# Optimization experiments

Measured on AMD Instinct MI355X. Metric: run time of the kernel, lower is better.

Reference implementation:

```python
import jax, jax.numpy as jnp
import numpy as np

N = 100000          # num nodes
E_C = 6_400_000     # connection edges
E_D = 400_000       # destination edges
F_IN = 5
H = 8
BN_EPS = 1e-5
L2_EPS = 1e-12


def setup_inputs() -> dict:
    key = jax.random.key(0)
    ks = jax.random.split(key, 16)
    d = {}
    d["x"] = jax.random.normal(ks[0], (N, F_IN), dtype=jnp.float32)
    d["edge_index_connections"] = jax.random.randint(ks[1], (2, E_C), 0, N, dtype=jnp.int64)
    d["edge_index_destinations"] = jax.random.randint(ks[2], (2, E_D), 0, N, dtype=jnp.int64)
    # SAGEConv weights: lin_l (neighbor aggregate), lin_r (root), no bias
    d["W1l"] = jax.random.normal(ks[3], (H, F_IN), jnp.float32) * 0.3
    d["W1r"] = jax.random.normal(ks[4], (H, F_IN), jnp.float32) * 0.3
    d["W2l"] = jax.random.normal(ks[5], (H, H), jnp.float32) * 0.3
    d["W2r"] = jax.random.normal(ks[6], (H, H), jnp.float32) * 0.3
    d["W3l"] = jax.random.normal(ks[7], (H, H), jnp.float32) * 0.3
    d["W3r"] = jax.random.normal(ks[8], (H, H), jnp.float32) * 0.3
    d["W4l"] = jax.random.normal(ks[9], (H, H), jnp.float32) * 0.3
    d["W4r"] = jax.random.normal(ks[10], (H, H), jnp.float32) * 0.3
    # LazyBatchNorm1d affine params (init gamma=1, beta=0)
    for i in range(1, 5):
        d[f"g{i}"] = jnp.ones((H,), jnp.float32)
        d[f"b{i}"] = jnp.zeros((H,), jnp.float32)
    return d


def _sage(x, ei, Wl, Wr):
    # PyG SAGEConv(mean aggr, normalize=True, bias=False):
    # out = lin_l(mean_{j in N(i)} x_j) + lin_r(x_i); then L2 normalize rows.
    src, dst = ei[0], ei[1]
    msgs = x[src]                                            # [E, F] gather
    s = jax.ops.segment_sum(msgs, dst, num_segments=N)       # [N, F]
    cnt = jax.ops.segment_sum(jnp.ones((ei.shape[1],), x.dtype), dst, num_segments=N)
    mean = s / jnp.maximum(cnt, 1.0)[:, None]                # zero for isolated nodes
    out = mean @ Wl.T + x @ Wr.T                             # [N, H]
    nrm = jnp.linalg.norm(out, axis=-1, keepdims=True)
    return out / jnp.maximum(nrm, L2_EPS)


def _bn(x, g, b):
    # BatchNorm1d in training mode: per-feature batch stats (biased variance)
    m = x.mean(axis=0)
    v = x.var(axis=0)
    return (x - m) * jax.lax.rsqrt(v + BN_EPS) * g + b


def reference(x, edge_index_connections, edge_index_destinations,
              W1l, W1r, W2l, W2r, W3l, W3r, W4l, W4r,
              g1, b1, g2, b2, g3, b3, g4, b4):
    eic = edge_index_connections
    eid = edge_index_destinations
    h = _bn(jax.nn.relu(_sage(x, eic, W1l, W1r)), g1, b1)
    # ITERATIONS_BEFORE_DESTINATION = 1 (conv4 + bn2)
    h = _bn(jax.nn.relu(_sage(h, eic, W4l, W4r)), g2, b2)
    # destination pass (conv2 + bn3)
    h = _bn(jax.nn.relu(_sage(h, eid, W2l, W2r)), g3, b3)
    # ITERATIONS_AFTER_DESTINATION = 2 (conv3 + bn4)
    for _ in range(2):
        h = _bn(jax.nn.relu(_sage(h, eic, W3l, W3r)), g4, b4)
    return h
```

## Files before the change

### kernel.cpp

```cpp
#include <hip/hip_runtime.h>
#include <hip/hip_fp16.h>

#define NN 100000
#define EC 6400000
#define ED 400000
#define BN_EPS 1e-5f
#define NSB ((NN + 255) >> 8)
#define NCH 256
#define CSR_CAP 19200
#define CHUNK_OF(E) (((((E) + NCH - 1) / NCH) + 3) & ~3)


__global__ __launch_bounds__(1024)
void hist_pass(const int* __restrict__ ei, int E, int* __restrict__ bhist) {
    __shared__ int h[NSB];
    for (int i = threadIdx.x; i < NSB; i += 1024) h[i] = 0;
    __syncthreads();
    int k = blockIdx.x;
    int chunk = CHUNK_OF(E);
    int beg = k * chunk, end = min(E, beg + chunk);
    for (int e = beg + threadIdx.x * 4; e < end; e += 1024 * 4) {
        int4 d4 = *(const int4*)&ei[E + e];
        atomicAdd(&h[d4.x >> 8], 1);
        atomicAdd(&h[d4.y >> 8], 1);
        atomicAdd(&h[d4.z >> 8], 1);
        atomicAdd(&h[d4.w >> 8], 1);
    }
    __syncthreads();
    for (int i = threadIdx.x; i < NSB; i += 1024) bhist[i * NCH + k] = h[i];
}

__global__ __launch_bounds__(256)
void row_scan(int* __restrict__ bhist, int* __restrict__ total) {
    int b = blockIdx.x;
    int* row = bhist + b * NCH;
    __shared__ int wsum[4];
    int lane = threadIdx.x & 63, w = threadIdx.x >> 6;
    int v = row[threadIdx.x];
    int x = v;
    #pragma unroll
    for (int sh = 1; sh < 64; sh <<= 1) { int y = __shfl_up(x, sh); if (lane >= sh) x += y; }
    if (lane == 63) wsum[w] = x;
    __syncthreads();
    int wb = 0;
    #pragma unroll
    for (int j = 0; j < 4; ++j) if (j < w) wb += wsum[j];
    row[threadIdx.x] = wb + x - v;
    if (threadIdx.x == 255) total[b] = wb + x;
}

__global__ void bucket_base(const int* __restrict__ total, int* __restrict__ bbase) {
    __shared__ int wsum[4];
    __shared__ int carry;
    if (threadIdx.x == 0) carry = 0;
    __syncthreads();
    int lane = threadIdx.x & 63, w = threadIdx.x >> 6;
    for (int s = 0; s < NSB; s += 256) {
        int idx = s + threadIdx.x;
        int v = (idx < NSB) ? total[idx] : 0;
        int x = v;
        #pragma unroll
        for (int sh = 1; sh < 64; sh <<= 1) { int y = __shfl_up(x, sh); if (lane >= sh) x += y; }
        if (lane == 63) wsum[w] = x;
        __syncthreads();
        int wb = 0;
        #pragma unroll
        for (int j = 0; j < 4; ++j) if (j < w) wb += wsum[j];
        int all = wsum[0] + wsum[1] + wsum[2] + wsum[3];
        if (idx < NSB) bbase[idx] = carry + wb + x - v;
        __syncthreads();
        if (threadIdx.x == 0) carry += all;
        __syncthreads();
    }
}

__global__ __launch_bounds__(1024)
void scatter_pairs(const int* __restrict__ ei, int E,
                   const int* __restrict__ bhist, const int* __restrict__ bbase,
                   unsigned* __restrict__ packed) {
    __shared__ int cur[NSB];
    int k = blockIdx.x;
    for (int b = threadIdx.x; b < NSB; b += 1024)
        cur[b] = bbase[b] + bhist[b * NCH + k];
    __syncthreads();
    int chunk = CHUNK_OF(E);
    int beg = k * chunk, end = min(E, beg + chunk);
    for (int e = beg + threadIdx.x * 4; e < end; e += 1024 * 4) {
        int4 s4 = *(const int4*)&ei[e];
        int4 d4 = *(const int4*)&ei[E + e];
        { int p = atomicAdd(&cur[d4.x >> 8], 1); packed[p] = (unsigned)s4.x | ((unsigned)(d4.x & 255) << 17); }
        { int p = atomicAdd(&cur[d4.y >> 8], 1); packed[p] = (unsigned)s4.y | ((unsigned)(d4.y & 255) << 17); }
        { int p = atomicAdd(&cur[d4.z >> 8], 1); packed[p] = (unsigned)s4.z | ((unsigned)(d4.z & 255) << 17); }
        { int p = atomicAdd(&cur[d4.w >> 8], 1); packed[p] = (unsigned)s4.w | ((unsigned)(d4.w & 255) << 17); }
    }
}

__global__ __launch_bounds__(256)
void sb_csr(const unsigned* __restrict__ packed,
            const int* __restrict__ bbase, const int* __restrict__ total,
            int* __restrict__ csr, int* __restrict__ offs, int* __restrict__ deg,
            float* __restrict__ inv) {
    __shared__ int h[256];
    __shared__ int loff[256];
    __shared__ int ws2[4];
    __shared__ int ebuf[CSR_CAP];
    int b = blockIdx.x;
    int ebeg = bbase[b], ecnt = total[b];
    int node0 = b << 8;
    int nn = min(256, NN - node0);
    h[threadIdx.x] = 0;
    __syncthreads();
    for (int e = threadIdx.x; e < ecnt; e += 256)
        atomicAdd(&h[packed[ebeg + e] >> 17], 1);
    __syncthreads();
    {
        int lane = threadIdx.x & 63, w = threadIdx.x >> 6;
        int v = h[threadIdx.x], x = v;
        #pragma unroll
        for (int sh = 1; sh < 64; sh <<= 1) { int y = __shfl_up(x, sh); if (lane >= sh) x += y; }
        if (lane == 63) ws2[w] = x;
        __syncthreads();
        int wb = 0;
        #pragma unroll
        for (int j = 0; j < 4; ++j) if (j < w) wb += ws2[j];
        int excl = wb + x - v;
        loff[threadIdx.x] = excl;
        if (threadIdx.x < nn) {
            int node = node0 + threadIdx.x;
            offs[node] = ebeg + excl;
            deg[node]  = v;
            inv[node]  = 1.0f / (float)(v > 1 ? v : 1);
        }
    }
    __syncthreads();
    if (ecnt <= CSR_CAP) {
        for (int e = threadIdx.x; e < ecnt; e += 256) {
            unsigned u = packed[ebeg + e];
            int p = atomicAdd(&loff[u >> 17], 1);
            ebuf[p] = (int)(u & 0x1FFFF);
        }
        __syncthreads();
        for (int e = threadIdx.x; e < ecnt; e += 256) csr[ebeg + e] = ebuf[e];
    } else {
        for (int e = threadIdx.x; e < ecnt; e += 256) {
            unsigned u = packed[ebeg + e];
            int p = atomicAdd(&loff[u >> 17], 1);
            csr[ebeg + p] = (int)(u & 0x1FFFF);
        }
    }
}

__global__ __launch_bounds__(256)
void prep_misc(const float* __restrict__ x, const float* __restrict__ W1l,
               const float* __restrict__ W1r, float* __restrict__ xp,
               __half* __restrict__ xp16,
               float* __restrict__ W1lp, float* __restrict__ W1rp) {
    int t = blockIdx.x * 256 + threadIdx.x;
    if (t < 64) {
        int f = t >> 3, k = t & 7;
        W1lp[t] = (k < 5) ? W1l[f * 5 + k] : 0.f;
        W1rp[t] = (k < 5) ? W1r[f * 5 + k] : 0.f;
    }
    for (int idx = t; idx < NN * 8; idx += gridDim.x * 256) {
        int f = idx & 7, i = idx >> 3;
        float v = (f < 5) ? x[i * 5 + f] : 0.f;
        xp[idx] = v;
        xp16[idx] = __float2half(v);
    }
}

template<bool APPLY_BN>
__global__ __launch_bounds__(256)
void sage_layer8(const float* __restrict__ hin,
                 const __half* __restrict__ hin16,
                 const float* __restrict__ stats_in,
                 const float* __restrict__ gin, const float* __restrict__ bin,
                 const int* __restrict__ offs, const int* __restrict__ deg,
                 const int* __restrict__ csr, const float* __restrict__ inv,
                 const float* __restrict__ Wl, const float* __restrict__ Wr,
                 float* __restrict__ hout, __half* __restrict__ hout16,
                 float* __restrict__ stats_out) {
    __shared__ float bl[16];
    int tid = threadIdx.x;
    if (tid < 16) bl[tid] = 0.f;
    __syncthreads();
    int wave = tid >> 6, lane = tid & 63, g = lane >> 3, f = lane & 7;

    float sc[8], sh[8];
    #pragma unroll
    for (int k = 0; k < 8; ++k) { sc[k] = 1.f; sh[k] = 0.f; }
    if constexpr (APPLY_BN) {
        #pragma unroll
        for (int k = 0; k < 8; ++k) {
            float m = stats_in[k * 16] * (1.f / NN);
            float v = stats_in[(8 + k) * 16] * (1.f / NN) - m * m;
            float is = rsqrtf(v + BN_EPS);
            sc[k] = gin[k] * is;
            sh[k] = bin[k] - m * sc[k];
        }
    }
    float wl[8], wr[8];
    #pragma unroll
    for (int k = 0; k < 8; ++k) { wl[k] = Wl[f * 8 + k]; wr[k] = Wr[f * 8 + k]; }

    float acc_r = 0.f, acc_r2 = 0.f;
    const int stride = gridDim.x * 32;
    for (int i0 = (blockIdx.x * 4 + wave) * 8; i0 < NN; i0 += stride) {
        int i = i0 + g;
        int ic = min(i, NN - 1);
        bool ok = (i < NN);
        int d = ok ? deg[ic] : 0;
        int o = offs[ic];
        float a0 = 0, a1 = 0, a2 = 0, a3 = 0, a4 = 0, a5 = 0, a6 = 0, a7 = 0;
        for (int b = 0; b < d; b += 8) {
            int e = b + f;
            int cv = csr[o + e];
            float m = (e < d) ? 1.f : 0.f;
            unsigned s = min((unsigned)cv & 0x1FFFFu, (unsigned)(NN - 1));
            uint4 rv = *(const uint4*)(hin16 + (size_t)s * 8);
            float2 p0 = __half22float2(*(const __half2*)&rv.x);
            float2 p1 = __half22float2(*(const __half2*)&rv.y);
            float2 p2 = __half22float2(*(const __half2*)&rv.z);
            float2 p3 = __half22float2(*(const __half2*)&rv.w);
            a0 = fmaf(p0.x, m, a0); a1 = fmaf(p0.y, m, a1);
            a2 = fmaf(p1.x, m, a2); a3 = fmaf(p1.y, m, a3);
            a4 = fmaf(p2.x, m, a4); a5 = fmaf(p2.y, m, a5);
            a6 = fmaf(p3.x, m, a6); a7 = fmaf(p3.y, m, a7);
        }
        #pragma unroll
        for (int msk = 1; msk < 8; msk <<= 1) {
            a0 += __shfl_xor(a0, msk); a1 += __shfl_xor(a1, msk);
            a2 += __shfl_xor(a2, msk); a3 += __shfl_xor(a3, msk);
            a4 += __shfl_xor(a4, msk); a5 += __shfl_xor(a5, msk);
            a6 += __shfl_xor(a6, msk); a7 += __shfl_xor(a7, msk);
        }
        float im = inv[ic];
        float dnz = (d > 0) ? 1.f : 0.f;
        const float4* hp = (const float4*)(hin + (size_t)ic * 8);
        float4 h0 = hp[0];
        float4 h1 = hp[1];
        float hk[8] = { h0.x, h0.y, h0.z, h0.w, h1.x, h1.y, h1.z, h1.w };
        float ac[8] = { a0, a1, a2, a3, a4, a5, a6, a7 };
        float y = 0.f;
        #pragma unroll
        for (int k = 0; k < 8; ++k) {
            float mk = fmaf(sc[k], ac[k] * im, sh[k] * dnz);
            float hh = fmaf(sc[k], hk[k], sh[k]);
            y = fmaf(mk, wl[k], y);
            y = fmaf(hh, wr[k], y);
        }
        float n2 = y * y;
        n2 += __shfl_xor(n2, 1);
        n2 += __shfl_xor(n2, 2);
        n2 += __shfl_xor(n2, 4);
        float z = y / fmaxf(sqrtf(n2), 1e-12f);
        float r = fmaxf(z, 0.f);
        r = ok ? r : 0.f;
        if (ok) {
            hout[(size_t)i * 8 + f] = r;
            hout16[(size_t)i * 8 + f] = __float2half(r);
        }
        acc_r += r;
        acc_r2 += r * r;
    }
    atomicAdd(&bl[f], acc_r);
    atomicAdd(&bl[8 + f], acc_r2);
    __syncthreads();
    if (tid < 16) atomicAdd(&stats_out[tid * 16], bl[tid]);
}

__global__ void apply_bn_out(const float* __restrict__ hin,
                             const float* __restrict__ stats,
                             const float* __restrict__ g, const float* __restrict__ b,
                             float* __restrict__ out) {
    int t = blockIdx.x * blockDim.x + threadIdx.x;
    if (t >= NN * 8) return;
    int f = t & 7;
    float m = stats[f * 16] * (1.0f / NN);
    float v = stats[(8 + f) * 16] * (1.0f / NN) - m * m;
    float sc = g[f] * rsqrtf(v + BN_EPS);
    float sh = b[f] - m * sc;
    out[t] = fmaf(hin[t], sc, sh);
}


static inline char* bump(char*& p, size_t bytes) {
    char* r = p;
    p += (bytes + 255) & ~(size_t)255;
    return r;
}

extern "C" void kernel_launch(void* const* d_in, const int* in_sizes, int n_in,
                              void* d_out, int out_size, void* d_ws, size_t ws_size,
                              hipStream_t stream) {
    const float* x   = (const float*)d_in[0];
    const int* eic   = (const int*)d_in[1];
    const int* eid   = (const int*)d_in[2];
    const float* W1l = (const float*)d_in[3];
    const float* W1r = (const float*)d_in[4];
    const float* W2l = (const float*)d_in[5];
    const float* W2r = (const float*)d_in[6];
    const float* W3l = (const float*)d_in[7];
    const float* W3r = (const float*)d_in[8];
    const float* W4l = (const float*)d_in[9];
    const float* W4r = (const float*)d_in[10];
    const float* g1 = (const float*)d_in[11];
    const float* b1 = (const float*)d_in[12];
    const float* g2 = (const float*)d_in[13];
    const float* b2 = (const float*)d_in[14];
    const float* g3 = (const float*)d_in[15];
    const float* b3 = (const float*)d_in[16];
    const float* g4 = (const float*)d_in[17];
    const float* b4 = (const float*)d_in[18];
    float* out = (float*)d_out;

    char* p = (char*)d_ws;
    float* stats   = (float*)bump(p, 5 * 256 * 4);
    size_t zero_bytes = (size_t)(p - (char*)d_ws);
    int*   bhist_c = (int*)  bump(p, (size_t)NSB * NCH * 4);
    int*   bhist_d = (int*)  bump(p, (size_t)NSB * NCH * 4);
    int*   total_c = (int*)  bump(p, NSB * 4);
    int*   bbase_c = (int*)  bump(p, NSB * 4);
    int*   total_d = (int*)  bump(p, NSB * 4);
    int*   bbase_d = (int*)  bump(p, NSB * 4);
    int*   offs_c  = (int*)  bump(p, NN * 4);
    int*   deg_c   = (int*)  bump(p, NN * 4);
    float* inv_c   = (float*)bump(p, NN * 4);
    int*   offs_d  = (int*)  bump(p, NN * 4);
    int*   deg_d   = (int*)  bump(p, NN * 4);
    float* inv_d   = (float*)bump(p, NN * 4);
    int*   csr_c   = (int*)  bump(p, ((size_t)EC + 64) * 4);
    int*   csr_d   = (int*)  bump(p, ((size_t)ED + 64) * 4);
    float* xp32    = (float*)bump(p, (size_t)NN * 8 * 4);
    __half* xp16   = (__half*)bump(p, (size_t)NN * 8 * 2);
    float* W1lp    = (float*)bump(p, 64 * 4);
    float* W1rp    = (float*)bump(p, 64 * 4);
    unsigned* packed_d = (unsigned*)bump(p, (size_t)ED * 4);
    char* pc = p;
    unsigned* packed_c = (unsigned*)bump(p, (size_t)EC * 4);
    char* pr = pc;
    float*  r_a   = (float*) bump(pr, (size_t)NN * 8 * 4);
    float*  r_b   = (float*) bump(pr, (size_t)NN * 8 * 4);
    __half* h16_a = (__half*)bump(pr, (size_t)NN * 8 * 2);
    __half* h16_b = (__half*)bump(pr, (size_t)NN * 8 * 2);
    (void)ws_size; (void)in_sizes; (void)n_in; (void)out_size; (void)packed_c;

    hipMemsetAsync(d_ws, 0, zero_bytes, stream);

    hist_pass<<<NCH, 1024, 0, stream>>>(eic, EC, bhist_c);
    hist_pass<<<NCH, 1024, 0, stream>>>(eid, ED, bhist_d);
    row_scan<<<NSB, 256, 0, stream>>>(bhist_c, total_c);
    row_scan<<<NSB, 256, 0, stream>>>(bhist_d, total_d);
    bucket_base<<<1, 256, 0, stream>>>(total_c, bbase_c);
    bucket_base<<<1, 256, 0, stream>>>(total_d, bbase_d);
    scatter_pairs<<<NCH, 1024, 0, stream>>>(eic, EC, bhist_c, bbase_c, packed_c);
    scatter_pairs<<<NCH, 1024, 0, stream>>>(eid, ED, bhist_d, bbase_d, packed_d);
    sb_csr<<<NSB, 256, 0, stream>>>(packed_c, bbase_c, total_c, csr_c, offs_c, deg_c, inv_c);
    sb_csr<<<NSB, 256, 0, stream>>>(packed_d, bbase_d, total_d, csr_d, offs_d, deg_d, inv_d);
    prep_misc<<<512, 256, 0, stream>>>(x, W1l, W1r, xp32, xp16, W1lp, W1rp);

    const int LB = 2048;
    sage_layer8<false><<<LB, 256, 0, stream>>>(
        xp32, xp16, nullptr, nullptr, nullptr,
        offs_c, deg_c, csr_c, inv_c, W1lp, W1rp, r_a, h16_a, stats + 0);
    sage_layer8<true><<<LB, 256, 0, stream>>>(
        r_a, h16_a, stats + 0, g1, b1,
        offs_c, deg_c, csr_c, inv_c, W4l, W4r, r_b, h16_b, stats + 256);
    sage_layer8<true><<<LB, 256, 0, stream>>>(
        r_b, h16_b, stats + 256, g2, b2,
        offs_d, deg_d, csr_d, inv_d, W2l, W2r, r_a, h16_a, stats + 512);
    sage_layer8<true><<<LB, 256, 0, stream>>>(
        r_a, h16_a, stats + 512, g3, b3,
        offs_c, deg_c, csr_c, inv_c, W3l, W3r, r_b, h16_b, stats + 768);
    sage_layer8<true><<<LB, 256, 0, stream>>>(
        r_b, h16_b, stats + 768, g4, b4,
        offs_c, deg_c, csr_c, inv_c, W3l, W3r, r_a, h16_a, stats + 1024);
    apply_bn_out<<<(NN * 8 + 255) / 256, 256, 0, stream>>>(r_a, stats + 1024, g4, b4, out);
}
```

Measured before the change: 625.3 us.

## Tile source features into LDS and bin edges by source tile for SAGE aggregation

Adds a preprocessing kernel that re-sorts each destination superblock's edges by 4096-row source tile. It packs the local destination index and the source offset into one word and records per-tile edge ranges. A new sage_spmm kernel, one block per 256 destination nodes, streams every fp16 source tile into LDS and accumulates neighbour sums with LDS float atomics. The goal is to replace random global gathers with LDS reads. In exchange, every block must re-read the whole feature table from L2. The kernel also uses about 73KB of LDS per block and launches only ~391 blocks, which limits occupancy. The destination-edge layer keeps the old CSR kernel.

```diff
diff --git a/kernel.cpp b/kernel.cpp
--- a/kernel.cpp
+++ b/kernel.cpp
@@ -8,6 +8,8 @@
 #define NSB ((NN + 255) >> 8)
 #define NCH 256
 #define CSR_CAP 19200
+#define TILE 4096
+#define NSUB ((NN + TILE - 1) / TILE)
 #define CHUNK_OF(E) (((((E) + NCH - 1) / NCH) + 3) & ~3)
 
 
@@ -92,6 +94,63 @@
         { int p = atomicAdd(&cur[d4.y >> 8], 1); packed[p] = (unsigned)s4.y | ((unsigned)(d4.y & 255) << 17); }
         { int p = atomicAdd(&cur[d4.z >> 8], 1); packed[p] = (unsigned)s4.z | ((unsigned)(d4.z & 255) << 17); }
         { int p = atomicAdd(&cur[d4.w >> 8], 1); packed[p] = (unsigned)s4.w | ((unsigned)(d4.w & 255) << 17); }
+    }
+}
+
+__global__ __launch_bounds__(256)
+void sb_group(const unsigned* __restrict__ packed,
+              const int* __restrict__ bbase, const int* __restrict__ total,
+              unsigned* __restrict__ packed2, int* __restrict__ gbin,
+              int* __restrict__ deg, float* __restrict__ inv) {
+    __shared__ int hn[256];
+    __shared__ int hb[NSUB];
+    __shared__ int boff[NSUB + 1];
+    __shared__ int cur[NSUB];
+    __shared__ unsigned ebuf[CSR_CAP];
+    int b = blockIdx.x;
+    int ebeg = bbase[b], ecnt = total[b];
+    int node0 = b << 8;
+    int nn = min(256, NN - node0);
+    hn[threadIdx.x] = 0;
+    if (threadIdx.x < NSUB) hb[threadIdx.x] = 0;
+    __syncthreads();
+    for (int e = threadIdx.x; e < ecnt; e += 256) {
+        unsigned u = packed[ebeg + e];
+        atomicAdd(&hn[u >> 17], 1);
+        atomicAdd(&hb[(u & 0x1FFFFu) >> 12], 1);
+    }
+    __syncthreads();
+    if (threadIdx.x == 0) {
+        int s = 0;
+        for (int i = 0; i < NSUB; ++i) { boff[i] = s; s += hb[i]; }
+        boff[NSUB] = s;
+    }
+    __syncthreads();
+    if (threadIdx.x <= NSUB) gbin[b * (NSUB + 1) + threadIdx.x] = ebeg + boff[threadIdx.x];
+    if (threadIdx.x < NSUB) cur[threadIdx.x] = boff[threadIdx.x];
+    if (threadIdx.x < nn) {
+        int node = node0 + threadIdx.x;
+        int d = hn[threadIdx.x];
+        deg[node] = d;
+        inv[node] = 1.0f / (float)(d > 1 ? d : 1);
+    }
+    __syncthreads();
+    if (ecnt <= CSR_CAP) {
+        for (int e = threadIdx.x; e < ecnt; e += 256) {
+            unsigned u = packed[ebeg + e];
+            int bin = (int)((u & 0x1FFFFu) >> 12);
+            int p = atomicAdd(&cur[bin], 1);
+            ebuf[p] = ((u >> 17) << 12) | (u & 0xFFFu);
+        }
+        __syncthreads();
+        for (int e = threadIdx.x; e < ecnt; e += 256) packed2[ebeg + e] = ebuf[e];
+    } else {
+        for (int e = threadIdx.x; e < ecnt; e += 256) {
+            unsigned u = packed[ebeg + e];
+            int bin = (int)((u & 0x1FFFFu) >> 12);
+            int p = atomicAdd(&cur[bin], 1);
+            packed2[ebeg + p] = ((u >> 17) << 12) | (u & 0xFFFu);
+        }
     }
 }
 
@@ -140,7 +199,7 @@
             ebuf[p] = (int)(u & 0x1FFFF);
         }
         __syncthreads();
-        for (int e = threadIdx.x; e < ecnt; e += 256) csr[ebeg + e] = ebuf[e];
+        for (int e = threadIdx.x; e < ecnt; e += 256) csr[ebeg + e] = (int)ebuf[e];
     } else {
         for (int e = threadIdx.x; e < ecnt; e += 256) {
             unsigned u = packed[ebeg + e];
@@ -167,6 +226,125 @@
         xp[idx] = v;
         xp16[idx] = __float2half(v);
     }
+}
+
+template<bool APPLY_BN>
+__global__ __launch_bounds__(256)
+void sage_spmm(const float* __restrict__ hin,
+               const __half* __restrict__ hin16,
+               const float* __restrict__ stats_in,
+               const float* __restrict__ gin, const float* __restrict__ bin,
+               const int* __restrict__ deg, const float* __restrict__ inv,
+               const int* __restrict__ gbin, const unsigned* __restrict__ packed2,
+               const float* __restrict__ Wl, const float* __restrict__ Wr,
+               float* __restrict__ hout, __half* __restrict__ hout16,
+               float* __restrict__ stats_out) {
+    __shared__ __align__(16) unsigned short tile[TILE * 8];
+    __shared__ float acc[256 * 9];
+    __shared__ float bl[16];
+    int tid = threadIdx.x;
+    int b = blockIdx.x;
+    int node0 = b << 8;
+    for (int i = tid; i < 256 * 9; i += 256) acc[i] = 0.f;
+    if (tid < 16) bl[tid] = 0.f;
+
+    float sc[8], sh[8];
+    #pragma unroll
+    for (int k = 0; k < 8; ++k) { sc[k] = 1.f; sh[k] = 0.f; }
+    if constexpr (APPLY_BN) {
+        #pragma unroll
+        for (int k = 0; k < 8; ++k) {
+            float m = stats_in[k * 16] * (1.f / NN);
+            float v = stats_in[(8 + k) * 16] * (1.f / NN) - m * m;
+            float is = rsqrtf(v + BN_EPS);
+            sc[k] = gin[k] * is;
+            sh[k] = bin[k] - m * sc[k];
+        }
+    }
+
+    const int* gb = gbin + b * (NSUB + 1);
+    for (int sub = 0; sub < NSUB; ++sub) {
+        int rs = sub * TILE;
+        int rows = min(TILE, NN - rs);
+        __syncthreads();
+        const uint4* gsrc = (const uint4*)(hin16 + (size_t)rs * 8);
+        uint4* lt = (uint4*)tile;
+        for (int r = tid; r < rows; r += 256) lt[r] = gsrc[r];
+        __syncthreads();
+        int e1 = gb[sub + 1];
+        for (int e = gb[sub] + tid; e < e1; e += 256) {
+            unsigned u = packed2[e];
+            int ld = (int)(u >> 12);
+            int sl = (int)(u & 0xFFFu);
+            uint4 rv = lt[sl];
+            float2 p0 = __half22float2(*(const __half2*)&rv.x);
+            float2 p1 = __half22float2(*(const __half2*)&rv.y);
+            float2 p2 = __half22float2(*(const __half2*)&rv.z);
+            float2 p3 = __half22float2(*(const __half2*)&rv.w);
+            float* a = &acc[ld * 9];
+            atomicAdd(a + 0, p0.x); atomicAdd(a + 1, p0.y);
+            atomicAdd(a + 2, p1.x); atomicAdd(a + 3, p1.y);
+            atomicAdd(a + 4, p2.x); atomicAdd(a + 5, p2.y);
+            atomicAdd(a + 6, p3.x); atomicAdd(a + 7, p3.y);
+        }
+    }
+    __syncthreads();
+
+    int nn = min(256, NN - node0);
+    bool ok = tid < nn;
+    int ii = node0 + (ok ? tid : (nn - 1));
+    int d = deg[ii];
+    float im = inv[ii];
+    float dnz = (d > 0) ? 1.f : 0.f;
+    const float4* hp = (const float4*)(hin + (size_t)ii * 8);
+    float4 h0 = hp[0], h1 = hp[1];
+    float hk[8] = { h0.x, h0.y, h0.z, h0.w, h1.x, h1.y, h1.z, h1.w };
+    float mk[8], hh[8];
+    #pragma unroll
+    for (int k = 0; k < 8; ++k) {
+        mk[k] = fmaf(sc[k], acc[tid * 9 + k] * im, sh[k] * dnz);
+        hh[k] = fmaf(sc[k], hk[k], sh[k]);
+    }
+    float y[8];
+    float n2 = 0.f;
+    #pragma unroll
+    for (int f = 0; f < 8; ++f) {
+        float t = 0.f;
+        #pragma unroll
+        for (int k = 0; k < 8; ++k) {
+            t = fmaf(mk[k], Wl[f * 8 + k], t);
+            t = fmaf(hh[k], Wr[f * 8 + k], t);
+        }
+        y[f] = t;
+        n2 += t * t;
+    }
+    float is = 1.f / fmaxf(sqrtf(n2), 1e-12f);
+    float rv[8];
+    #pragma unroll
+    for (int f = 0; f < 8; ++f) rv[f] = ok ? fmaxf(y[f] * is, 0.f) : 0.f;
+    if (ok) {
+        float4 o0 = { rv[0], rv[1], rv[2], rv[3] };
+        float4 o1 = { rv[4], rv[5], rv[6], rv[7] };
+        float4* op = (float4*)(hout + (size_t)ii * 8);
+        op[0] = o0; op[1] = o1;
+        __half2 q0 = __floats2half2_rn(rv[0], rv[1]);
+        __half2 q1 = __floats2half2_rn(rv[2], rv[3]);
+        __half2 q2 = __floats2half2_rn(rv[4], rv[5]);
+        __half2 q3 = __floats2half2_rn(rv[6], rv[7]);
+        uint4 hq;
+        hq.x = *(unsigned*)&q0; hq.y = *(unsigned*)&q1;
+        hq.z = *(unsigned*)&q2; hq.w = *(unsigned*)&q3;
+        *(uint4*)(hout16 + (size_t)ii * 8) = hq;
+    }
+    #pragma unroll
+    for (int f = 0; f < 8; ++f) {
+        float s1 = rv[f], s2 = rv[f] * rv[f];
+        #pragma unroll
+        for (int m = 1; m < 64; m <<= 1) { s1 += __shfl_xor(s1, m); s2 += __shfl_xor(s2, m); }
+        if ((tid & 63) == 0) { atomicAdd(&bl[f], s1); atomicAdd(&bl[8 + f], s2); }
+    }
+    __syncthreads();
+    if (tid < 16) atomicAdd(&stats_out[tid * 16], bl[tid]);
 }
 
 template<bool APPLY_BN>
@@ -323,13 +501,13 @@
     int*   bbase_c = (int*)  bump(p, NSB * 4);
     int*   total_d = (int*)  bump(p, NSB * 4);
     int*   bbase_d = (int*)  bump(p, NSB * 4);
-    int*   offs_c  = (int*)  bump(p, NN * 4);
+    int*   gbin_c  = (int*)  bump(p, (size_t)NSB * (NSUB + 1) * 4);
     int*   deg_c   = (int*)  bump(p, NN * 4);
     float* inv_c   = (float*)bump(p, NN * 4);
     int*   offs_d  = (int*)  bump(p, NN * 4);
     int*   deg_d   = (int*)  bump(p, NN * 4);
     float* inv_d   = (float*)bump(p, NN * 4);
-    int*   csr_c   = (int*)  bump(p, ((size_t)EC + 64) * 4);
+    unsigned* packed2_c = (unsigned*)bump(p, (size_t)EC * 4);
     int*   csr_d   = (int*)  bump(p, ((size_t)ED + 64) * 4);
     float* xp32    = (float*)bump(p, (size_t)NN * 8 * 4);
     __half* xp16   = (__half*)bump(p, (size_t)NN * 8 * 2);
@@ -343,7 +521,7 @@
     float*  r_b   = (float*) bump(pr, (size_t)NN * 8 * 4);
     __half* h16_a = (__half*)bump(pr, (size_t)NN * 8 * 2);
     __half* h16_b = (__half*)bump(pr, (size_t)NN * 8 * 2);
-    (void)ws_size; (void)in_sizes; (void)n_in; (void)out_size; (void)packed_c;
+    (void)ws_size; (void)in_sizes; (void)n_in; (void)out_size;
 
     hipMemsetAsync(d_ws, 0, zero_bytes, stream);
 
@@ -355,25 +533,24 @@
     bucket_base<<<1, 256, 0, stream>>>(total_d, bbase_d);
     scatter_pairs<<<NCH, 1024, 0, stream>>>(eic, EC, bhist_c, bbase_c, packed_c);
     scatter_pairs<<<NCH, 1024, 0, stream>>>(eid, ED, bhist_d, bbase_d, packed_d);
-    sb_csr<<<NSB, 256, 0, stream>>>(packed_c, bbase_c, total_c, csr_c, offs_c, deg_c, inv_c);
+    sb_group<<<NSB, 256, 0, stream>>>(packed_c, bbase_c, total_c, packed2_c, gbin_c, deg_c, inv_c);
     sb_csr<<<NSB, 256, 0, stream>>>(packed_d, bbase_d, total_d, csr_d, offs_d, deg_d, inv_d);
     prep_misc<<<512, 256, 0, stream>>>(x, W1l, W1r, xp32, xp16, W1lp, W1rp);
 
-    const int LB = 2048;
-    sage_layer8<false><<<LB, 256, 0, stream>>>(
+    sage_spmm<false><<<NSB, 256, 0, stream>>>(
         xp32, xp16, nullptr, nullptr, nullptr,
-        offs_c, deg_c, csr_c, inv_c, W1lp, W1rp, r_a, h16_a, stats + 0);
-    sage_layer8<true><<<LB, 256, 0, stream>>>(
+        deg_c, inv_c, gbin_c, packed2_c, W1lp, W1rp, r_a, h16_a, stats + 0);
+    sage_spmm<true><<<NSB, 256, 0, stream>>>(
         r_a, h16_a, stats + 0, g1, b1,
-        offs_c, deg_c, csr_c, inv_c, W4l, W4r, r_b, h16_b, stats + 256);
-    sage_layer8<true><<<LB, 256, 0, stream>>>(
+        deg_c, inv_c, gbin_c, packed2_c, W4l, W4r, r_b, h16_b, stats + 256);
+    sage_layer8<true><<<2048, 256, 0, stream>>>(
         r_b, h16_b, stats + 256, g2, b2,
         offs_d, deg_d, csr_d, inv_d, W2l, W2r, r_a, h16_a, stats + 512);
-    sage_layer8<true><<<LB, 256, 0, stream>>>(
+    sage_spmm<true><<<NSB, 256, 0, stream>>>(
         r_a, h16_a, stats + 512, g3, b3,
-        offs_c, deg_c, csr_c, inv_c, W3l, W3r, r_b, h16_b, stats + 768);
-    sage_layer8<true><<<LB, 256, 0, stream>>>(
+        deg_c, inv_c, gbin_c, packed2_c, W3l, W3r, r_b, h16_b, stats + 768);
+    sage_spmm<true><<<NSB, 256, 0, stream>>>(
         r_b, h16_b, stats + 768, g4, b4,
-        offs_c, deg_c, csr_c, inv_c, W3l, W3r, r_a, h16_a, stats + 1024);
+        deg_c, inv_c, gbin_c, packed2_c, W3l, W3r, r_a, h16_a, stats + 1024);
     apply_bn_out<<<(NN * 8 + 255) / 256, 256, 0, stream>>>(r_a, stats + 1024, g4, b4, out);
 }
```

After: 1.892 ms. 203% more time.

## Replace counting-sort CSR build with fixed-capacity bucket scatter via global atomics

Applied to the files above, without the earlier changes.

Drops the histogram, row-scan and bucket-base kernels. Edges are scattered directly into fixed-capacity per-64-node sub-buckets using global atomic cursors, then per-256-node blocks build CSR from four sub-buckets. Connection and destination graphs and the input prep are merged into two launches. This cuts launches and one pass over the edge list, at the cost of global atomic contention and padded memory. Overflow beyond the capacity is clamped, which silently corrupts results if any sub-bucket exceeds it.

```diff
diff --git a/kernel.cpp b/kernel.cpp
--- a/kernel.cpp
+++ b/kernel.cpp
@@ -6,112 +6,103 @@
 #define ED 400000
 #define BN_EPS 1e-5f
 #define NSB ((NN + 255) >> 8)
+#define NSBS 1564
 #define NCH 256
 #define CSR_CAP 19200
+#define SCAP_C 5120
+#define BK_C (4 * SCAP_C)
+#define SCAP_D 512
+#define BK_D (4 * SCAP_D)
 #define CHUNK_OF(E) (((((E) + NCH - 1) / NCH) + 3) & ~3)
 
 
 __global__ __launch_bounds__(1024)
-void hist_pass(const int* __restrict__ ei, int E, int* __restrict__ bhist) {
-    __shared__ int h[NSB];
-    for (int i = threadIdx.x; i < NSB; i += 1024) h[i] = 0;
-    __syncthreads();
-    int k = blockIdx.x;
-    int chunk = CHUNK_OF(E);
-    int beg = k * chunk, end = min(E, beg + chunk);
-    for (int e = beg + threadIdx.x * 4; e < end; e += 1024 * 4) {
-        int4 d4 = *(const int4*)&ei[E + e];
-        atomicAdd(&h[d4.x >> 8], 1);
-        atomicAdd(&h[d4.y >> 8], 1);
-        atomicAdd(&h[d4.z >> 8], 1);
-        atomicAdd(&h[d4.w >> 8], 1);
-    }
-    __syncthreads();
-    for (int i = threadIdx.x; i < NSB; i += 1024) bhist[i * NCH + k] = h[i];
+void scatter_prep(const int* __restrict__ eic, const int* __restrict__ eid,
+                  int* __restrict__ gcur_c, unsigned* __restrict__ packed_c,
+                  int* __restrict__ gcur_d, unsigned* __restrict__ packed_d,
+                  const float* __restrict__ x, const float* __restrict__ W1l,
+                  const float* __restrict__ W1r, float* __restrict__ xp,
+                  __half* __restrict__ xp16,
+                  float* __restrict__ W1lp, float* __restrict__ W1rp) {
+    int blk = blockIdx.x;
+    if (blk < 2 * NCH) {
+        bool isC = blk < NCH;
+        const int* ei = isC ? eic : eid;
+        int E = isC ? EC : ED;
+        int* gcur = isC ? gcur_c : gcur_d;
+        unsigned* packed = isC ? packed_c : packed_d;
+        int SC = isC ? SCAP_C : SCAP_D;
+        int k = isC ? blk : blk - NCH;
+        int chunk = CHUNK_OF(E);
+        int beg = k * chunk, end = min(E, beg + chunk);
+        for (int e = beg + threadIdx.x * 4; e < end; e += 1024 * 4) {
+            int4 s4 = *(const int4*)&ei[e];
+            int4 d4 = *(const int4*)&ei[E + e];
+            { int sb = d4.x >> 6; int p = min(atomicAdd(&gcur[sb], 1), SC - 1);
+              packed[(size_t)sb * SC + p] = (unsigned)s4.x | ((unsigned)(d4.x & 255) << 17); }
+            { int sb = d4.y >> 6; int p = min(atomicAdd(&gcur[sb], 1), SC - 1);
+              packed[(size_t)sb * SC + p] = (unsigned)s4.y | ((unsigned)(d4.y & 255) << 17); }
+            { int sb = d4.z >> 6; int p = min(atomicAdd(&gcur[sb], 1), SC - 1);
+              packed[(size_t)sb * SC + p] = (unsigned)s4.z | ((unsigned)(d4.z & 255) << 17); }
+            { int sb = d4.w >> 6; int p = min(atomicAdd(&gcur[sb], 1), SC - 1);
+              packed[(size_t)sb * SC + p] = (unsigned)s4.w | ((unsigned)(d4.w & 255) << 17); }
+        }
+    } else {
+        int pb = blk - 2 * NCH;
+        int t = pb * 1024 + threadIdx.x;
+        if (t < 64) {
+            int f = t >> 3, k = t & 7;
+            W1lp[t] = (k < 5) ? W1l[f * 5 + k] : 0.f;
+            W1rp[t] = (k < 5) ? W1r[f * 5 + k] : 0.f;
+        }
+        for (int idx = t; idx < NN * 8; idx += 32 * 1024) {
+            int f = idx & 7, i = idx >> 3;
+            float v = (f < 5) ? x[i * 5 + f] : 0.f;
+            xp[idx] = v;
+            xp16[idx] = __float2half(v);
+        }
+    }
 }
 
 __global__ __launch_bounds__(256)
-void row_scan(int* __restrict__ bhist, int* __restrict__ total) {
-    int b = blockIdx.x;
-    int* row = bhist + b * NCH;
-    __shared__ int wsum[4];
-    int lane = threadIdx.x & 63, w = threadIdx.x >> 6;
-    int v = row[threadIdx.x];
-    int x = v;
-    #pragma unroll
-    for (int sh = 1; sh < 64; sh <<= 1) { int y = __shfl_up(x, sh); if (lane >= sh) x += y; }
-    if (lane == 63) wsum[w] = x;
-    __syncthreads();
-    int wb = 0;
-    #pragma unroll
-    for (int j = 0; j < 4; ++j) if (j < w) wb += wsum[j];
-    row[threadIdx.x] = wb + x - v;
-    if (threadIdx.x == 255) total[b] = wb + x;
-}
-
-__global__ void bucket_base(const int* __restrict__ total, int* __restrict__ bbase) {
-    __shared__ int wsum[4];
-    __shared__ int carry;
-    if (threadIdx.x == 0) carry = 0;
-    __syncthreads();
-    int lane = threadIdx.x & 63, w = threadIdx.x >> 6;
-    for (int s = 0; s < NSB; s += 256) {
-        int idx = s + threadIdx.x;
-        int v = (idx < NSB) ? total[idx] : 0;
-        int x = v;
-        #pragma unroll
-        for (int sh = 1; sh < 64; sh <<= 1) { int y = __shfl_up(x, sh); if (lane >= sh) x += y; }
-        if (lane == 63) wsum[w] = x;
-        __syncthreads();
-        int wb = 0;
-        #pragma unroll
-        for (int j = 0; j < 4; ++j) if (j < w) wb += wsum[j];
-        int all = wsum[0] + wsum[1] + wsum[2] + wsum[3];
-        if (idx < NSB) bbase[idx] = carry + wb + x - v;
-        __syncthreads();
-        if (threadIdx.x == 0) carry += all;
-        __syncthreads();
-    }
-}
-
-__global__ __launch_bounds__(1024)
-void scatter_pairs(const int* __restrict__ ei, int E,
-                   const int* __restrict__ bhist, const int* __restrict__ bbase,
-                   unsigned* __restrict__ packed) {
-    __shared__ int cur[NSB];
-    int k = blockIdx.x;
-    for (int b = threadIdx.x; b < NSB; b += 1024)
-        cur[b] = bbase[b] + bhist[b * NCH + k];
-    __syncthreads();
-    int chunk = CHUNK_OF(E);
-    int beg = k * chunk, end = min(E, beg + chunk);
-    for (int e = beg + threadIdx.x * 4; e < end; e += 1024 * 4) {
-        int4 s4 = *(const int4*)&ei[e];
-        int4 d4 = *(const int4*)&ei[E + e];
-        { int p = atomicAdd(&cur[d4.x >> 8], 1); packed[p] = (unsigned)s4.x | ((unsigned)(d4.x & 255) << 17); }
-        { int p = atomicAdd(&cur[d4.y >> 8], 1); packed[p] = (unsigned)s4.y | ((unsigned)(d4.y & 255) << 17); }
-        { int p = atomicAdd(&cur[d4.z >> 8], 1); packed[p] = (unsigned)s4.z | ((unsigned)(d4.z & 255) << 17); }
-        { int p = atomicAdd(&cur[d4.w >> 8], 1); packed[p] = (unsigned)s4.w | ((unsigned)(d4.w & 255) << 17); }
-    }
-}
-
-__global__ __launch_bounds__(256)
-void sb_csr(const unsigned* __restrict__ packed,
-            const int* __restrict__ bbase, const int* __restrict__ total,
-            int* __restrict__ csr, int* __restrict__ offs, int* __restrict__ deg,
-            float* __restrict__ inv) {
+void csr2(const unsigned* __restrict__ packed_c, const int* __restrict__ gcur_c,
+          int* __restrict__ csr_c, int* __restrict__ offs_c,
+          int* __restrict__ deg_c, float* __restrict__ inv_c,
+          const unsigned* __restrict__ packed_d, const int* __restrict__ gcur_d,
+          int* __restrict__ csr_d, int* __restrict__ offs_d,
+          int* __restrict__ deg_d, float* __restrict__ inv_d) {
+    int blk = blockIdx.x;
+    bool isC = blk < NSB;
+    const unsigned* packed = isC ? packed_c : packed_d;
+    const int* gcur = isC ? gcur_c : gcur_d;
+    int* csr  = isC ? csr_c : csr_d;
+    int* offs = isC ? offs_c : offs_d;
+    int* deg  = isC ? deg_c : deg_d;
+    float* inv = isC ? inv_c : inv_d;
+    int SC = isC ? SCAP_C : SCAP_D;
+    int BK = isC ? BK_C : BK_D;
+    int b = isC ? blk : blk - NSB;
+
     __shared__ int h[256];
     __shared__ int loff[256];
     __shared__ int ws2[4];
     __shared__ int ebuf[CSR_CAP];
-    int b = blockIdx.x;
-    int ebeg = bbase[b], ecnt = total[b];
     int node0 = b << 8;
     int nn = min(256, NN - node0);
+    int B0 = b * BK;
+    int cnt[4];
+    #pragma unroll
+    for (int j = 0; j < 4; ++j) cnt[j] = gcur[4 * b + j];
+    int ecnt = cnt[0] + cnt[1] + cnt[2] + cnt[3];
+
     h[threadIdx.x] = 0;
     __syncthreads();
-    for (int e = threadIdx.x; e < ecnt; e += 256)
-        atomicAdd(&h[packed[ebeg + e] >> 17], 1);
+    #pragma unroll
+    for (int j = 0; j < 4; ++j) {
+        const unsigned* pp = packed + (size_t)(4 * b + j) * SC;
+        for (int e = threadIdx.x; e < cnt[j]; e += 256)
+            atomicAdd(&h[pp[e] >> 17], 1);
+    }
     __syncthreads();
     {
         int lane = threadIdx.x & 63, w = threadIdx.x >> 6;
@@ -127,45 +118,34 @@
         loff[threadIdx.x] = excl;
         if (threadIdx.x < nn) {
             int node = node0 + threadIdx.x;
-            offs[node] = ebeg + excl;
+            offs[node] = B0 + excl;
             deg[node]  = v;
             inv[node]  = 1.0f / (float)(v > 1 ? v : 1);
         }
     }
     __syncthreads();
     if (ecnt <= CSR_CAP) {
-        for (int e = threadIdx.x; e < ecnt; e += 256) {
-            unsigned u = packed[ebeg + e];
-            int p = atomicAdd(&loff[u >> 17], 1);
-            ebuf[p] = (int)(u & 0x1FFFF);
+        #pragma unroll
+        for (int j = 0; j < 4; ++j) {
+            const unsigned* pp = packed + (size_t)(4 * b + j) * SC;
+            for (int e = threadIdx.x; e < cnt[j]; e += 256) {
+                unsigned u = pp[e];
+                int p = atomicAdd(&loff[u >> 17], 1);
+                ebuf[p] = (int)(u & 0x1FFFF);
+            }
         }
         __syncthreads();
-        for (int e = threadIdx.x; e < ecnt; e += 256) csr[ebeg + e] = ebuf[e];
+        for (int e = threadIdx.x; e < ecnt; e += 256) csr[B0 + e] = ebuf[e];
     } else {
-        for (int e = threadIdx.x; e < ecnt; e += 256) {
-            unsigned u = packed[ebeg + e];
-            int p = atomicAdd(&loff[u >> 17], 1);
-            csr[ebeg + p] = (int)(u & 0x1FFFF);
-        }
-    }
-}
-
-__global__ __launch_bounds__(256)
-void prep_misc(const float* __restrict__ x, const float* __restrict__ W1l,
-               const float* __restrict__ W1r, float* __restrict__ xp,
-               __half* __restrict__ xp16,
-               float* __restrict__ W1lp, float* __restrict__ W1rp) {
-    int t = blockIdx.x * 256 + threadIdx.x;
-    if (t < 64) {
-        int f = t >> 3, k = t & 7;
-        W1lp[t] = (k < 5) ? W1l[f * 5 + k] : 0.f;
-        W1rp[t] = (k < 5) ? W1r[f * 5 + k] : 0.f;
-    }
-    for (int idx = t; idx < NN * 8; idx += gridDim.x * 256) {
-        int f = idx & 7, i = idx >> 3;
-        float v = (f < 5) ? x[i * 5 + f] : 0.f;
-        xp[idx] = v;
-        xp16[idx] = __float2half(v);
+        #pragma unroll
+        for (int j = 0; j < 4; ++j) {
+            const unsigned* pp = packed + (size_t)(4 * b + j) * SC;
+            for (int e = threadIdx.x; e < cnt[j]; e += 256) {
+                unsigned u = pp[e];
+                int p = atomicAdd(&loff[u >> 17], 1);
+                csr[B0 + p] = (int)(u & 0x1FFFF);
+            }
+        }
     }
 }
 
@@ -316,48 +296,38 @@
 
     char* p = (char*)d_ws;
     float* stats   = (float*)bump(p, 5 * 256 * 4);
+    int*   gcur_c  = (int*)  bump(p, NSBS * 4);
+    int*   gcur_d  = (int*)  bump(p, NSBS * 4);
     size_t zero_bytes = (size_t)(p - (char*)d_ws);
-    int*   bhist_c = (int*)  bump(p, (size_t)NSB * NCH * 4);
-    int*   bhist_d = (int*)  bump(p, (size_t)NSB * NCH * 4);
-    int*   total_c = (int*)  bump(p, NSB * 4);
-    int*   bbase_c = (int*)  bump(p, NSB * 4);
-    int*   total_d = (int*)  bump(p, NSB * 4);
-    int*   bbase_d = (int*)  bump(p, NSB * 4);
     int*   offs_c  = (int*)  bump(p, NN * 4);
     int*   deg_c   = (int*)  bump(p, NN * 4);
     float* inv_c   = (float*)bump(p, NN * 4);
     int*   offs_d  = (int*)  bump(p, NN * 4);
     int*   deg_d   = (int*)  bump(p, NN * 4);
     float* inv_d   = (float*)bump(p, NN * 4);
-    int*   csr_c   = (int*)  bump(p, ((size_t)EC + 64) * 4);
-    int*   csr_d   = (int*)  bump(p, ((size_t)ED + 64) * 4);
+    int*   csr_c   = (int*)  bump(p, (size_t)NSB * BK_C * 4);
+    int*   csr_d   = (int*)  bump(p, (size_t)NSB * BK_D * 4);
     float* xp32    = (float*)bump(p, (size_t)NN * 8 * 4);
     __half* xp16   = (__half*)bump(p, (size_t)NN * 8 * 2);
     float* W1lp    = (float*)bump(p, 64 * 4);
     float* W1rp    = (float*)bump(p, 64 * 4);
-    unsigned* packed_d = (unsigned*)bump(p, (size_t)ED * 4);
+    unsigned* packed_d = (unsigned*)bump(p, (size_t)NSB * BK_D * 4);
     char* pc = p;
-    unsigned* packed_c = (unsigned*)bump(p, (size_t)EC * 4);
+    unsigned* packed_c = (unsigned*)bump(p, (size_t)NSB * BK_C * 4);
     char* pr = pc;
     float*  r_a   = (float*) bump(pr, (size_t)NN * 8 * 4);
     float*  r_b   = (float*) bump(pr, (size_t)NN * 8 * 4);
     __half* h16_a = (__half*)bump(pr, (size_t)NN * 8 * 2);
     __half* h16_b = (__half*)bump(pr, (size_t)NN * 8 * 2);
-    (void)ws_size; (void)in_sizes; (void)n_in; (void)out_size; (void)packed_c;
+    (void)ws_size; (void)in_sizes; (void)n_in; (void)out_size;
 
     hipMemsetAsync(d_ws, 0, zero_bytes, stream);
-
-    hist_pass<<<NCH, 1024, 0, stream>>>(eic, EC, bhist_c);
-    hist_pass<<<NCH, 1024, 0, stream>>>(eid, ED, bhist_d);
-    row_scan<<<NSB, 256, 0, stream>>>(bhist_c, total_c);
-    row_scan<<<NSB, 256, 0, stream>>>(bhist_d, total_d);
-    bucket_base<<<1, 256, 0, stream>>>(total_c, bbase_c);
-    bucket_base<<<1, 256, 0, stream>>>(total_d, bbase_d);
-    scatter_pairs<<<NCH, 1024, 0, stream>>>(eic, EC, bhist_c, bbase_c, packed_c);
-    scatter_pairs<<<NCH, 1024, 0, stream>>>(eid, ED, bhist_d, bbase_d, packed_d);
-    sb_csr<<<NSB, 256, 0, stream>>>(packed_c, bbase_c, total_c, csr_c, offs_c, deg_c, inv_c);
-    sb_csr<<<NSB, 256, 0, stream>>>(packed_d, bbase_d, total_d, csr_d, offs_d, deg_d, inv_d);
-    prep_misc<<<512, 256, 0, stream>>>(x, W1l, W1r, xp32, xp16, W1lp, W1rp);
+    scatter_prep<<<2 * NCH + 32, 1024, 0, stream>>>(
+        eic, eid, gcur_c, packed_c, gcur_d, packed_d,
+        x, W1l, W1r, xp32, xp16, W1lp, W1rp);
+    csr2<<<2 * NSB, 256, 0, stream>>>(
+        packed_c, gcur_c, csr_c, offs_c, deg_c, inv_c,
+        packed_d, gcur_d, csr_d, offs_d, deg_d, inv_d);
 
     const int LB = 2048;
     sage_layer8<false><<<LB, 256, 0, stream>>>(
```

After: 1.479 ms. 2.37x slower.
